# Optimization experiments

Hardware: AMD Instinct MI355X
Metric: run time of the kernel (lower is better)

## Reference

```python
import jax, jax.numpy as jnp
import numpy as np
import math

DIM_V = 512
NUM_HEADS = 8
LN_EPS = 1e-5


def _layer_norm(x, g, b):
    mu = jnp.mean(x, axis=-1, keepdims=True)
    var = jnp.mean(jnp.square(x - mu), axis=-1, keepdims=True)
    return (x - mu) * jax.lax.rsqrt(var + LN_EPS) * g + b


def setup_inputs() -> dict:
    key = jax.random.key(0)
    ks = jax.random.split(key, 12)
    B, Nq, Nk, Dq, Dk, Dv = 16, 1024, 1024, 512, 512, DIM_V
    s_q = 1.0 / math.sqrt(Dq)
    s_k = 1.0 / math.sqrt(Dk)
    s_v = 1.0 / math.sqrt(Dv)
    return {
        "Q": jax.random.normal(ks[0], (B, Nq, Dq), jnp.float32),
        "K": jax.random.normal(ks[1], (B, Nk, Dk), jnp.float32),
        "Wq": jax.random.normal(ks[2], (Dq, Dv), jnp.float32) * s_q,
        "bq": jnp.zeros((Dv,), jnp.float32),
        "Wk": jax.random.normal(ks[3], (Dk, Dv), jnp.float32) * s_k,
        "bk": jnp.zeros((Dv,), jnp.float32),
        "Wv": jax.random.normal(ks[4], (Dk, Dv), jnp.float32) * s_k,
        "bv": jnp.zeros((Dv,), jnp.float32),
        "Wo": jax.random.normal(ks[5], (Dv, Dv), jnp.float32) * s_v,
        "bo": jnp.zeros((Dv,), jnp.float32),
        "g0": jnp.ones((Dv,), jnp.float32),
        "b0": jnp.zeros((Dv,), jnp.float32),
        "g1": jnp.ones((Dv,), jnp.float32),
        "b1": jnp.zeros((Dv,), jnp.float32),
    }


def reference(Q, K, Wq, bq, Wk, bk, Wv, bv, Wo, bo, g0, b0, g1, b1):
    B, Nq, _ = Q.shape
    H = NUM_HEADS
    hd = DIM_V // H
    Qp = Q @ Wq + bq            # [B, Nq, Dv]
    Kp = K @ Wk + bk            # [B, Nk, Dv]
    Vp = K @ Wv + bv            # [B, Nk, Dv]
    # split heads: [B, N, H, hd]
    Qh = Qp.reshape(B, Nq, H, hd)
    Kh = Kp.reshape(B, -1, H, hd)
    Vh = Vp.reshape(B, -1, H, hd)
    # NOTE: original scales by sqrt(dim_V), not sqrt(head_dim)
    scores = jnp.einsum("bqhd,bkhd->bhqk", Qh, Kh) / math.sqrt(DIM_V)
    A = jax.nn.softmax(scores, axis=-1)          # [B, H, Nq, Nk]
    Oh = Qh + jnp.einsum("bhqk,bkhd->bqhd", A, Vh)  # residual on projected Q
    O = Oh.reshape(B, Nq, DIM_V)
    O = _layer_norm(O, g0, b0)
    O = O + jax.nn.relu(O @ Wo + bo)
    O = _layer_norm(O, g1, b1)
    return O
```

## Files before the change

### kernel.cpp

```cpp
#include <hip/hip_runtime.h>
#include <hip/hip_bf16.h>

typedef float f32x4 __attribute__((ext_vector_type(4)));
typedef float f32x16 __attribute__((ext_vector_type(16)));
typedef __bf16 bf16x8 __attribute__((ext_vector_type(8)));
typedef __bf16 bf16x4 __attribute__((ext_vector_type(4)));

#define MFMA(a, b, c) __builtin_amdgcn_mfma_f32_16x16x32_bf16(a, b, c, 0, 0, 0)
#define MFMA32(a, b, c) __builtin_amdgcn_mfma_f32_32x32x16_bf16(a, b, c, 0, 0, 0)
#define AS1 __attribute__((address_space(1)))
#define AS3 __attribute__((address_space(3)))

__device__ __forceinline__ void gload16(const void* g, void* l) {
    __builtin_amdgcn_global_load_lds((const AS1 unsigned int*)g, (AS3 unsigned int*)l, 16, 0, 0);
}

__device__ __forceinline__ unsigned short f2bf(float f) {
    union { float f; unsigned u; } x{f};
    unsigned r = x.u + 0x7FFFu + ((x.u >> 16) & 1u);
    return (unsigned short)(r >> 16);
}
__device__ __forceinline__ float bf2f(unsigned short u) {
    union { unsigned u; float f; } x; x.u = ((unsigned)u) << 16; return x.f;
}
__device__ __forceinline__ unsigned pkbf(float a, float b) {
    union { __bf16 h[2]; unsigned u; } r;
    r.h[0] = (__bf16)a; r.h[1] = (__bf16)b;
    return r.u;
}

__global__ __launch_bounds__(256) void k_transpose4(const float* W0, const float* W1,
                                                    const float* W2, const float* W3,
                                                    unsigned short* T0, unsigned short* T1,
                                                    unsigned short* T2, unsigned short* T3) {
    __shared__ float T[64][65];
    int sel = blockIdx.x >> 6, tile = blockIdx.x & 63;
    const float* W = sel == 0 ? W0 : sel == 1 ? W1 : sel == 2 ? W2 : W3;
    unsigned short* Wt = sel == 0 ? T0 : sel == 1 ? T1 : sel == 2 ? T2 : T3;
    int k0 = (tile >> 3) * 64, n0 = (tile & 7) * 64;
    int tid = threadIdx.x;
    for (int it = 0; it < 16; ++it) {
        int id = it * 256 + tid;
        int r = id >> 6, c = id & 63;
        T[r][c] = W[(k0 + r) * 512 + n0 + c];
    }
    __syncthreads();
    for (int it = 0; it < 16; ++it) {
        int id = it * 256 + tid;
        int r = id >> 6, c = id & 63;
        Wt[(n0 + r) * 512 + k0 + c] = f2bf(T[c][r]);
    }
}

template <int MODE>
__global__ __launch_bounds__(256) void k_gemmF(const float* __restrict__ A,
                                               const unsigned short* __restrict__ Bt,
                                               const float* __restrict__ bias,
                                               void* __restrict__ outp,
                                               float scale) {
    __shared__ __align__(16) float AbS[2][4096];
    __shared__ __align__(16) unsigned short BbS[2][4096];
    const int tid = threadIdx.x;
    const int lane = tid & 63, w = tid >> 6;
    int ib = blockIdx.x;
    const int mt = (ib & 7) | ((ib >> 5) << 3), nt = (ib >> 3) & 3;
    const int m0 = mt * 128, n0 = nt * 128;
    const int wm = (w >> 1) * 64, wn = (w & 1) * 64;
    const int l15 = lane & 15, l4 = lane >> 4;

    const f32x4 vz = {0.f, 0.f, 0.f, 0.f};
    f32x4 acc[4][4];
    for (int i = 0; i < 4; ++i)
        for (int j = 0; j < 4; ++j) acc[i][j] = vz;

    const float* Abase = A + (size_t)m0 * 512;
    const unsigned short* Bbase = Bt + (size_t)n0 * 512;

    auto STAGE = [&](int ks, int p) {
        int kk = ks * 32;
        #pragma unroll
        for (int it = 0; it < 4; ++it) {
            int id = it * 256 + tid;
            int r = id >> 3, cc = id & 7, g = cc ^ (r & 7);
            gload16(Abase + r * 512 + kk + g * 4, &AbS[p][(it * 256 + w * 64) * 4]);
        }
        #pragma unroll
        for (int it = 0; it < 2; ++it) {
            int id = it * 256 + tid;
            int r = id >> 2, x = id & 3, c = x ^ (r & 3);
            gload16(Bbase + r * 512 + kk + c * 8, &BbS[p][(it * 256 + w * 64) * 8]);
        }
    };

    STAGE(0, 0);
    __syncthreads();
    for (int ks = 0; ks < 16; ++ks) {
        int p = ks & 1;
        if (ks < 15) STAGE(ks + 1, p ^ 1);
        bf16x8 af[4], bfr[4];
        #pragma unroll
        for (int i = 0; i < 4; ++i) {
            int r = wm + i * 16 + l15;
            int pc0 = (2 * l4) ^ (r & 7);
            const float* Af = &AbS[p][r * 32];
            f32x4 a0 = *(const f32x4*)(Af + pc0 * 4);
            f32x4 a1 = *(const f32x4*)(Af + (pc0 ^ 1) * 4);
            af[i] = bf16x8{(__bf16)a0[0], (__bf16)a0[1], (__bf16)a0[2], (__bf16)a0[3],
                           (__bf16)a1[0], (__bf16)a1[1], (__bf16)a1[2], (__bf16)a1[3]};
        }
        #pragma unroll
        for (int j = 0; j < 4; ++j) {
            int r = wn + j * 16 + l15, pc = l4 ^ (r & 3);
            bfr[j] = *(const bf16x8*)&BbS[p][r * 32 + pc * 8];
        }
        __builtin_amdgcn_s_setprio(1);
        #pragma unroll
        for (int i = 0; i < 4; ++i)
            #pragma unroll
            for (int j = 0; j < 4; ++j)
                acc[i][j] = MFMA(af[i], bfr[j], acc[i][j]);
        __builtin_amdgcn_s_setprio(0);
        __syncthreads();
    }

    float bn[4];
    for (int j = 0; j < 4; ++j) bn[j] = bias[n0 + wn + j * 16 + l15];

    if constexpr (MODE == 0) {
        unsigned short* out = (unsigned short*)outp;
        for (int i = 0; i < 4; ++i)
            for (int j = 0; j < 4; ++j)
                for (int rg = 0; rg < 4; ++rg) {
                    int m = m0 + wm + i * 16 + l4 * 4 + rg;
                    int n = n0 + wn + j * 16 + l15;
                    out[(size_t)m * 512 + n] = f2bf((acc[i][j][rg] + bn[j]) * scale);
                }
    } else {
        unsigned short* T = (unsigned short*)&AbS[0][0] + w * 4096;
        __syncthreads();
        for (int i = 0; i < 4; ++i)
            for (int j = 0; j < 4; ++j)
                for (int rg = 0; rg < 4; ++rg) {
                    int ml = i * 16 + l4 * 4 + rg;
                    int nl = j * 16 + l15;
                    int pc = (ml >> 3) ^ (nl & 7);
                    T[nl * 64 + pc * 8 + (ml & 7)] = f2bf(acc[i][j][rg] + bn[j]);
                }
        unsigned short* out = (unsigned short*)outp;
        int b = (m0 + wm) >> 10;
        int key0 = (m0 + wm) & 1023;
        for (int it = 0; it < 8; ++it) {
            int ch = it * 64 + lane;
            int nl = ch >> 3, c = ch & 7, pc = c ^ (nl & 7);
            int4 v = *(const int4*)&T[nl * 64 + pc * 8];
            int d = n0 + wn + nl;
            *(int4*)(out + ((size_t)b * 512 + d) * 1024 + key0 + c * 8) = v;
        }
    }
}

__global__ __launch_bounds__(256, 4) void k_attn32(const unsigned short* __restrict__ Qs,
                                                   const unsigned short* __restrict__ Kp,
                                                   const unsigned short* __restrict__ VpT,
                                                   unsigned short* __restrict__ O1b) {
    __shared__ __align__(16) unsigned short sm[16384];
    const int tid = threadIdx.x, lane = tid & 63, w = tid >> 6;
    const int l31 = lane & 31, hi = lane >> 5;
    int i = blockIdx.x;
    const int xcd = i & 7, jj = i >> 3;
    const int qt = jj & 7, bhl = jj >> 3;
    const int bh = xcd * 16 + bhl;
    const int h = bh & 7, b = bh >> 3;
    const int qrow = b * 1024 + qt * 128 + w * 32 + l31;

    const unsigned short* Ksrc = Kp + (size_t)(b * 1024) * 512 + h * 64;
    const unsigned short* Vsrc = VpT + (size_t)(b * 512 + h * 64) * 1024;
    const unsigned short* qptr = Qs + (size_t)qrow * 512 + h * 64;

    bf16x8 qf[4];
    #pragma unroll
    for (int ks = 0; ks < 4; ++ks)
        qf[ks] = *(const bf16x8*)(qptr + ks * 16 + hi * 8);

    f32x16 acc0, acc1;
    #pragma unroll
    for (int r = 0; r < 16; ++r) { acc0[r] = 0.f; acc1[r] = 0.f; }
    float ls = 0.f;

    auto STAGE = [&](int kv, int p) {
        #pragma unroll
        for (int it = 0; it < 2; ++it) {
            int id = it * 256 + tid;
            int r = id >> 3, x = id & 7, c = x ^ (r & 7);
            unsigned short* ldsb = sm + p * 4096 + (it * 256 + w * 64) * 8;
            gload16(Ksrc + (size_t)(kv * 64 + r) * 512 + c * 8, ldsb);
            gload16(Vsrc + (size_t)r * 1024 + kv * 64 + c * 8, ldsb + 8192);
        }
    };

    STAGE(0, 0);
    __syncthreads();
    for (int kv = 0; kv < 16; ++kv) {
        int p = kv & 1;
        if (kv < 15) STAGE(kv + 1, p ^ 1);
        const unsigned short* Kl = sm + p * 4096;
        const unsigned short* Vl = sm + 8192 + p * 4096;
        const int rsw = (l31 & 7);

        f32x16 s0, s1;
        #pragma unroll
        for (int r = 0; r < 16; ++r) { s0[r] = 0.f; s1[r] = 0.f; }
        __builtin_amdgcn_s_setprio(1);
        #pragma unroll
        for (int ks = 0; ks < 4; ++ks) {
            int c = (2 * ks + hi) ^ rsw;
            bf16x8 kf0 = *(const bf16x8*)&Kl[l31 * 64 + c * 8];
            s0 = MFMA32(kf0, qf[ks], s0);
            bf16x8 kf1 = *(const bf16x8*)&Kl[(32 + l31) * 64 + c * 8];
            s1 = MFMA32(kf1, qf[ks], s1);
        }
        __builtin_amdgcn_s_setprio(0);

        unsigned We[8], Wf[8];
        #pragma unroll
        for (int g = 0; g < 4; ++g) {
            float e0 = __builtin_amdgcn_exp2f(s0[4 * g + 0]);
            float e1 = __builtin_amdgcn_exp2f(s0[4 * g + 1]);
            float e2 = __builtin_amdgcn_exp2f(s0[4 * g + 2]);
            float e3 = __builtin_amdgcn_exp2f(s0[4 * g + 3]);
            float f0 = __builtin_amdgcn_exp2f(s1[4 * g + 0]);
            float f1 = __builtin_amdgcn_exp2f(s1[4 * g + 1]);
            float f2 = __builtin_amdgcn_exp2f(s1[4 * g + 2]);
            float f3 = __builtin_amdgcn_exp2f(s1[4 * g + 3]);
            ls += ((e0 + e1) + (e2 + e3)) + ((f0 + f1) + (f2 + f3));
            We[2 * g + 0] = pkbf(e0, e1); We[2 * g + 1] = pkbf(e2, e3);
            Wf[2 * g + 0] = pkbf(f0, f1); Wf[2 * g + 1] = pkbf(f2, f3);
        }
        bf16x8 pf[4];
        #pragma unroll
        for (int src = 0; src < 2; ++src) {
            const unsigned* W = src == 0 ? We : Wf;
            #pragma unroll
            for (int k2 = 0; k2 < 2; ++k2) {
                unsigned A0 = W[4 * k2 + 0], A1 = W[4 * k2 + 1];
                unsigned B0 = W[4 * k2 + 2], B1 = W[4 * k2 + 3];
                unsigned cross0 = __shfl_xor(hi ? A0 : B0, 32);
                unsigned cross1 = __shfl_xor(hi ? A1 : B1, 32);
                union { unsigned w[4]; bf16x8 v; } r;
                r.w[0] = hi ? cross0 : A0;
                r.w[1] = hi ? cross1 : A1;
                r.w[2] = hi ? B0 : cross0;
                r.w[3] = hi ? B1 : cross1;
                pf[src * 2 + k2] = r.v;
            }
        }

        __builtin_amdgcn_s_setprio(1);
        #pragma unroll
        for (int ks = 0; ks < 4; ++ks) {
            int c = (2 * ks + hi) ^ rsw;
            bf16x8 vf0 = *(const bf16x8*)&Vl[l31 * 64 + c * 8];
            acc0 = MFMA32(vf0, pf[ks], acc0);
            bf16x8 vf1 = *(const bf16x8*)&Vl[(32 + l31) * 64 + c * 8];
            acc1 = MFMA32(vf1, pf[ks], acc1);
        }
        __builtin_amdgcn_s_setprio(0);
        __syncthreads();
    }

    ls += __shfl_xor(ls, 32);
    float linv = 1.0f / ls;
    const float invscale = 15.6841306f;
    unsigned short* orow = O1b + (size_t)qrow * 512 + h * 64;
    #pragma unroll
    for (int g = 0; g < 4; ++g) {
        {
            int d0 = 8 * g + 4 * hi;
            bf16x4 qres = *(const bf16x4*)(qptr + d0);
            bf16x4 ov;
            ov[0] = (__bf16)((float)qres[0] * invscale + acc0[4 * g + 0] * linv);
            ov[1] = (__bf16)((float)qres[1] * invscale + acc0[4 * g + 1] * linv);
            ov[2] = (__bf16)((float)qres[2] * invscale + acc0[4 * g + 2] * linv);
            ov[3] = (__bf16)((float)qres[3] * invscale + acc0[4 * g + 3] * linv);
            *(bf16x4*)(orow + d0) = ov;
        }
        {
            int d0 = 32 + 8 * g + 4 * hi;
            bf16x4 qres = *(const bf16x4*)(qptr + d0);
            bf16x4 ov;
            ov[0] = (__bf16)((float)qres[0] * invscale + acc1[4 * g + 0] * linv);
            ov[1] = (__bf16)((float)qres[1] * invscale + acc1[4 * g + 1] * linv);
            ov[2] = (__bf16)((float)qres[2] * invscale + acc1[4 * g + 2] * linv);
            ov[3] = (__bf16)((float)qres[3] * invscale + acc1[4 * g + 3] * linv);
            *(bf16x4*)(orow + d0) = ov;
        }
    }
}

__global__ __launch_bounds__(256) void k_ln_bf(const unsigned short* __restrict__ in,
                                               unsigned short* __restrict__ outb,
                                               const float* __restrict__ g,
                                               const float* __restrict__ bt) {
    int row = blockIdx.x * 4 + (threadIdx.x >> 6);
    int lane = threadIdx.x & 63;
    const unsigned short* x = in + (size_t)row * 512 + lane * 8;
    bf16x8 v = *(const bf16x8*)x;
    float f[8];
    for (int j = 0; j < 8; ++j) f[j] = (float)v[j];
    float s1 = 0.f, s2 = 0.f;
    for (int j = 0; j < 8; ++j) { s1 += f[j]; s2 += f[j] * f[j]; }
    for (int off = 32; off; off >>= 1) {
        s1 += __shfl_xor(s1, off);
        s2 += __shfl_xor(s2, off);
    }
    float mu = s1 * (1.f / 512.f);
    float var = s2 * (1.f / 512.f) - mu * mu;
    float rs = rsqrtf(var + 1e-5f);
    float4 ga = *(const float4*)(g + lane * 8), gb = *(const float4*)(g + lane * 8 + 4);
    float4 ba = *(const float4*)(bt + lane * 8), bb = *(const float4*)(bt + lane * 8 + 4);
    float gg[8] = {ga.x, ga.y, ga.z, ga.w, gb.x, gb.y, gb.z, gb.w};
    float bv[8] = {ba.x, ba.y, ba.z, ba.w, bb.x, bb.y, bb.z, bb.w};
    bf16x8 y;
    for (int j = 0; j < 8; ++j) y[j] = (__bf16)((f[j] - mu) * rs * gg[j] + bv[j]);
    *(bf16x8*)(outb + (size_t)row * 512 + lane * 8) = y;
}

__global__ __launch_bounds__(512, 2) void k_gemm2ln(const unsigned short* __restrict__ A,
                                                    const unsigned short* __restrict__ Bt,
                                                    const float* __restrict__ bias,
                                                    const float* __restrict__ g1,
                                                    const float* __restrict__ b1,
                                                    float* __restrict__ out) {
    __shared__ __align__(16) unsigned short Ab[2][2048];
    __shared__ __align__(16) unsigned short Bb[2][16384];
    __shared__ float part[64][4][2];
    __shared__ float stats[64][2];
    const int tid = threadIdx.x, lane = tid & 63, w = tid >> 6;
    const int l15 = lane & 15, l4 = lane >> 4;
    const int m0 = blockIdx.x * 64;
    const int wm = (w >> 2) * 32, wn = (w & 3) * 128;

    const f32x4 vz = {0.f, 0.f, 0.f, 0.f};
    f32x4 acc[2][8];
    for (int i = 0; i < 2; ++i)
        for (int j = 0; j < 8; ++j) acc[i][j] = vz;

    const unsigned short* Abase = A + (size_t)m0 * 512;

    auto STAGE = [&](int ks, int p) {
        int kk = ks * 32;
        for (int it = 0; it < 4; ++it) {
            int id = it * 512 + tid;
            int r = id >> 2, x = id & 3, c = x ^ (r & 3);
            gload16(Bt + r * 512 + kk + c * 8, &Bb[p][(it * 512 + w * 64) * 8]);
        }
        if (w < 4) {
            int id = w * 64 + lane;
            int r = id >> 2, x = id & 3, c = x ^ (r & 3);
            gload16(Abase + r * 512 + kk + c * 8, &Ab[p][(w * 64) * 8]);
        }
    };

    STAGE(0, 0);
    __syncthreads();
    for (int ks = 0; ks < 16; ++ks) {
        int p = ks & 1;
        if (ks < 15) STAGE(ks + 1, p ^ 1);
        bf16x8 af[2], bfr[8];
        for (int i = 0; i < 2; ++i) {
            int r = wm + i * 16 + l15, pc = l4 ^ (r & 3);
            af[i] = *(const bf16x8*)&Ab[p][r * 32 + pc * 8];
        }
        for (int j = 0; j < 8; ++j) {
            int r = wn + j * 16 + l15, pc = l4 ^ (r & 3);
            bfr[j] = *(const bf16x8*)&Bb[p][r * 32 + pc * 8];
        }
        __builtin_amdgcn_s_setprio(1);
        for (int i = 0; i < 2; ++i)
            for (int j = 0; j < 8; ++j)
                acc[i][j] = MFMA(af[i], bfr[j], acc[i][j]);
        __builtin_amdgcn_s_setprio(0);
        __syncthreads();
    }

    float bn[8], gv[8], bv2[8];
    for (int j = 0; j < 8; ++j) {
        int n = wn + j * 16 + l15;
        bn[j] = bias[n]; gv[j] = g1[n]; bv2[j] = b1[n];
    }
    f32x4 s1v[2], s2v[2];
    for (int i = 0; i < 2; ++i) { s1v[i] = vz; s2v[i] = vz; }
    for (int i = 0; i < 2; ++i)
        for (int j = 0; j < 8; ++j)
            for (int rg = 0; rg < 4; ++rg) {
                int row = m0 + wm + i * 16 + l4 * 4 + rg;
                int n = wn + j * 16 + l15;
                float z = acc[i][j][rg] + bn[j];
                z = z > 0.f ? z : 0.f;
                float v = bf2f(A[(size_t)row * 512 + n]) + z;
                acc[i][j][rg] = v;
                s1v[i][rg] += v;
                s2v[i][rg] += v * v;
            }
    for (int i = 0; i < 2; ++i)
        for (int rg = 0; rg < 4; ++rg) {
            float a = s1v[i][rg], c = s2v[i][rg];
            for (int off = 1; off < 16; off <<= 1) {
                a += __shfl_xor(a, off);
                c += __shfl_xor(c, off);
            }
            s1v[i][rg] = a; s2v[i][rg] = c;
        }
    if (l15 == 0)
        for (int i = 0; i < 2; ++i)
            for (int rg = 0; rg < 4; ++rg) {
                int rl = wm + i * 16 + l4 * 4 + rg;
                part[rl][w & 3][0] = s1v[i][rg];
                part[rl][w & 3][1] = s2v[i][rg];
            }
    __syncthreads();
    if (tid < 64) {
        float a = 0.f, c = 0.f;
        for (int q = 0; q < 4; ++q) { a += part[tid][q][0]; c += part[tid][q][1]; }
        float mu = a * (1.f / 512.f);
        float var = c * (1.f / 512.f) - mu * mu;
        stats[tid][0] = mu;
        stats[tid][1] = rsqrtf(var + 1e-5f);
    }
    __syncthreads();
    for (int i = 0; i < 2; ++i)
        for (int rg = 0; rg < 4; ++rg) {
            int rl = wm + i * 16 + l4 * 4 + rg;
            float mu = stats[rl][0], rs = stats[rl][1];
            for (int j = 0; j < 8; ++j) {
                int n = wn + j * 16 + l15;
                out[(size_t)(m0 + rl) * 512 + n] = (acc[i][j][rg] - mu) * rs * gv[j] + bv2[j];
            }
        }
}

extern "C" void kernel_launch(void* const* d_in, const int* in_sizes, int n_in,
                              void* d_out, int out_size, void* d_ws, size_t ws_size,
                              hipStream_t stream) {
    const float* Q  = (const float*)d_in[0];
    const float* K  = (const float*)d_in[1];
    const float* Wq = (const float*)d_in[2];
    const float* bq = (const float*)d_in[3];
    const float* Wk = (const float*)d_in[4];
    const float* bk = (const float*)d_in[5];
    const float* Wv = (const float*)d_in[6];
    const float* bv = (const float*)d_in[7];
    const float* Wo = (const float*)d_in[8];
    const float* bo = (const float*)d_in[9];
    const float* g0 = (const float*)d_in[10];
    const float* b0 = (const float*)d_in[11];
    const float* g1 = (const float*)d_in[12];
    const float* b1 = (const float*)d_in[13];
    float* out = (float*)d_out;

    const size_t SZ_BF = (size_t)16384 * 512 * 2;
    const size_t SZ_W  = (size_t)512 * 512 * 2;
    char* p = (char*)d_ws;
    unsigned short* Wqt = (unsigned short*)p; p += SZ_W;
    unsigned short* Wkt = (unsigned short*)p; p += SZ_W;
    unsigned short* Wvt = (unsigned short*)p; p += SZ_W;
    unsigned short* Wot = (unsigned short*)p; p += SZ_W;
    unsigned short* Qsc = (unsigned short*)p; p += SZ_BF;
    unsigned short* Kp  = (unsigned short*)p; p += SZ_BF;
    unsigned short* VpT = (unsigned short*)p; p += SZ_BF;
    unsigned short* A1b = (unsigned short*)p; p += SZ_BF;
    unsigned short* X0b = (unsigned short*)p; p += SZ_BF;

    k_transpose4<<<256, 256, 0, stream>>>(Wq, Wk, Wv, Wo, Wqt, Wkt, Wvt, Wot);

    const float scale2 = 0.063758718f;
    k_gemmF<0><<<512, 256, 0, stream>>>(Q, Wqt, bq, Qsc, scale2);
    k_gemmF<0><<<512, 256, 0, stream>>>(K, Wkt, bk, Kp, 1.0f);
    k_gemmF<1><<<512, 256, 0, stream>>>(K, Wvt, bv, VpT, 1.0f);

    k_attn32<<<1024, 256, 0, stream>>>(Qsc, Kp, VpT, A1b);

    k_ln_bf<<<4096, 256, 0, stream>>>(A1b, X0b, g0, b0);
    k_gemm2ln<<<256, 512, 0, stream>>>(X0b, Wot, bo, g1, b1, out);
}
```

Baseline: 154.6 us.

## Merge QKV projections into one launch; attention waves process 64 query rows

Folds the three projection GEMM launches into a single 1536-block kernel that picks its input, weights and output by block index, which removes launch gaps and fills the device better. The attention kernel moves to 128-thread blocks where each wave handles two 32-row query groups, so every K/V fragment read from LDS feeds twice as many MFMAs. Each block also starts its KV loop at a rotated tile offset so concurrent blocks read different K/V tiles. In exchange the attention kernel uses more registers per wave and has fewer waves per block to hide load latency.

Result: faster. 142.5 us (-7.8%).

```diff
diff --git a/kernel.cpp b/kernel.cpp
--- a/kernel.cpp
+++ b/kernel.cpp
@@ -27,6 +27,42 @@
     union { __bf16 h[2]; unsigned u; } r;
     r.h[0] = (__bf16)a; r.h[1] = (__bf16)b;
     return r.u;
+}
+
+__device__ __forceinline__ void softmax_pack(const f32x16& s0, const f32x16& s1,
+                                             float& ls, int hi, bf16x8* pf) {
+    unsigned We[8], Wf[8];
+    #pragma unroll
+    for (int g = 0; g < 4; ++g) {
+        float e0 = __builtin_amdgcn_exp2f(s0[4 * g + 0]);
+        float e1 = __builtin_amdgcn_exp2f(s0[4 * g + 1]);
+        float e2 = __builtin_amdgcn_exp2f(s0[4 * g + 2]);
+        float e3 = __builtin_amdgcn_exp2f(s0[4 * g + 3]);
+        float f0 = __builtin_amdgcn_exp2f(s1[4 * g + 0]);
+        float f1 = __builtin_amdgcn_exp2f(s1[4 * g + 1]);
+        float f2 = __builtin_amdgcn_exp2f(s1[4 * g + 2]);
+        float f3 = __builtin_amdgcn_exp2f(s1[4 * g + 3]);
+        ls += ((e0 + e1) + (e2 + e3)) + ((f0 + f1) + (f2 + f3));
+        We[2 * g + 0] = pkbf(e0, e1); We[2 * g + 1] = pkbf(e2, e3);
+        Wf[2 * g + 0] = pkbf(f0, f1); Wf[2 * g + 1] = pkbf(f2, f3);
+    }
+    #pragma unroll
+    for (int src = 0; src < 2; ++src) {
+        const unsigned* W = src == 0 ? We : Wf;
+        #pragma unroll
+        for (int k2 = 0; k2 < 2; ++k2) {
+            unsigned A0 = W[4 * k2 + 0], A1 = W[4 * k2 + 1];
+            unsigned B0 = W[4 * k2 + 2], B1 = W[4 * k2 + 3];
+            unsigned cross0 = __shfl_xor(hi ? A0 : B0, 32);
+            unsigned cross1 = __shfl_xor(hi ? A1 : B1, 32);
+            union { unsigned w[4]; bf16x8 v; } r;
+            r.w[0] = hi ? cross0 : A0;
+            r.w[1] = hi ? cross1 : A1;
+            r.w[2] = hi ? B0 : cross0;
+            r.w[3] = hi ? B1 : cross1;
+            pf[src * 2 + k2] = r.v;
+        }
+    }
 }
 
 __global__ __launch_bounds__(256) void k_transpose4(const float* W0, const float* W1,
@@ -52,17 +88,28 @@
     }
 }
 
-template <int MODE>
-__global__ __launch_bounds__(256) void k_gemmF(const float* __restrict__ A,
-                                               const unsigned short* __restrict__ Bt,
-                                               const float* __restrict__ bias,
-                                               void* __restrict__ outp,
-                                               float scale) {
+__global__ __launch_bounds__(256) void k_proj(const float* __restrict__ Qf,
+                                              const float* __restrict__ Kf,
+                                              const unsigned short* __restrict__ Wqt,
+                                              const unsigned short* __restrict__ Wkt,
+                                              const unsigned short* __restrict__ Wvt,
+                                              const float* __restrict__ bq,
+                                              const float* __restrict__ bk,
+                                              const float* __restrict__ bv,
+                                              unsigned short* __restrict__ Qsc,
+                                              unsigned short* __restrict__ Kpo,
+                                              unsigned short* __restrict__ VpT,
+                                              float scale2) {
     __shared__ __align__(16) float AbS[2][4096];
     __shared__ __align__(16) unsigned short BbS[2][4096];
     const int tid = threadIdx.x;
     const int lane = tid & 63, w = tid >> 6;
-    int ib = blockIdx.x;
+    const int sel = blockIdx.x >> 9;
+    int ib = blockIdx.x & 511;
+    const float* A = sel == 0 ? Qf : Kf;
+    const unsigned short* Bt = sel == 0 ? Wqt : sel == 1 ? Wkt : Wvt;
+    const float* bias = sel == 0 ? bq : sel == 1 ? bk : bv;
+    const float scale = sel == 0 ? scale2 : 1.0f;
     const int mt = (ib & 7) | ((ib >> 5) << 3), nt = (ib >> 3) & 3;
     const int m0 = mt * 128, n0 = nt * 128;
     const int wm = (w >> 1) * 64, wn = (w & 1) * 64;
@@ -126,8 +173,8 @@
     float bn[4];
     for (int j = 0; j < 4; ++j) bn[j] = bias[n0 + wn + j * 16 + l15];
 
-    if constexpr (MODE == 0) {
-        unsigned short* out = (unsigned short*)outp;
+    if (sel < 2) {
+        unsigned short* out = sel == 0 ? Qsc : Kpo;
         for (int i = 0; i < 4; ++i)
             for (int j = 0; j < 4; ++j)
                 for (int rg = 0; rg < 4; ++rg) {
@@ -146,7 +193,6 @@
                     int pc = (ml >> 3) ^ (nl & 7);
                     T[nl * 64 + pc * 8 + (ml & 7)] = f2bf(acc[i][j][rg] + bn[j]);
                 }
-        unsigned short* out = (unsigned short*)outp;
         int b = (m0 + wm) >> 10;
         int key0 = (m0 + wm) & 1023;
         for (int it = 0; it < 8; ++it) {
@@ -154,12 +200,12 @@
             int nl = ch >> 3, c = ch & 7, pc = c ^ (nl & 7);
             int4 v = *(const int4*)&T[nl * 64 + pc * 8];
             int d = n0 + wn + nl;
-            *(int4*)(out + ((size_t)b * 512 + d) * 1024 + key0 + c * 8) = v;
-        }
-    }
-}
-
-__global__ __launch_bounds__(256, 4) void k_attn32(const unsigned short* __restrict__ Qs,
+            *(int4*)(VpT + ((size_t)b * 512 + d) * 1024 + key0 + c * 8) = v;
+        }
+    }
+}
+
+__global__ __launch_bounds__(128, 2) void k_attn64(const unsigned short* __restrict__ Qs,
                                                    const unsigned short* __restrict__ Kp,
                                                    const unsigned short* __restrict__ VpT,
                                                    unsigned short* __restrict__ O1b) {
@@ -167,132 +213,125 @@
     const int tid = threadIdx.x, lane = tid & 63, w = tid >> 6;
     const int l31 = lane & 31, hi = lane >> 5;
     int i = blockIdx.x;
-    const int xcd = i & 7, jj = i >> 3;
-    const int qt = jj & 7, bhl = jj >> 3;
+    const int xcd = i & 7, r2 = i >> 3;
+    const int bhl = r2 & 15, qt = r2 >> 4;
     const int bh = xcd * 16 + bhl;
     const int h = bh & 7, b = bh >> 3;
-    const int qrow = b * 1024 + qt * 128 + w * 32 + l31;
+    const int q0 = b * 1024 + qt * 128 + w * 64;
+    const int kv0 = (qt * 3 + bhl * 5) & 15;
 
     const unsigned short* Ksrc = Kp + (size_t)(b * 1024) * 512 + h * 64;
     const unsigned short* Vsrc = VpT + (size_t)(b * 512 + h * 64) * 1024;
-    const unsigned short* qptr = Qs + (size_t)qrow * 512 + h * 64;
-
-    bf16x8 qf[4];
+    const unsigned short* qptrA = Qs + (size_t)(q0 + l31) * 512 + h * 64;
+    const unsigned short* qptrB = qptrA + (size_t)32 * 512;
+
+    bf16x8 qfA[4], qfB[4];
     #pragma unroll
-    for (int ks = 0; ks < 4; ++ks)
-        qf[ks] = *(const bf16x8*)(qptr + ks * 16 + hi * 8);
-
-    f32x16 acc0, acc1;
+    for (int ks = 0; ks < 4; ++ks) {
+        qfA[ks] = *(const bf16x8*)(qptrA + ks * 16 + hi * 8);
+        qfB[ks] = *(const bf16x8*)(qptrB + ks * 16 + hi * 8);
+    }
+
+    f32x16 accA0, accA1, accB0, accB1;
     #pragma unroll
-    for (int r = 0; r < 16; ++r) { acc0[r] = 0.f; acc1[r] = 0.f; }
-    float ls = 0.f;
-
-    auto STAGE = [&](int kv, int p) {
-        #pragma unroll
-        for (int it = 0; it < 2; ++it) {
-            int id = it * 256 + tid;
+    for (int r = 0; r < 16; ++r) { accA0[r] = 0.f; accA1[r] = 0.f; accB0[r] = 0.f; accB1[r] = 0.f; }
+    float lsA = 0.f, lsB = 0.f;
+
+    auto STAGE = [&](int j, int p) {
+        int t = (j + kv0) & 15;
+        #pragma unroll
+        for (int it = 0; it < 4; ++it) {
+            int id = it * 128 + tid;
             int r = id >> 3, x = id & 7, c = x ^ (r & 7);
-            unsigned short* ldsb = sm + p * 4096 + (it * 256 + w * 64) * 8;
-            gload16(Ksrc + (size_t)(kv * 64 + r) * 512 + c * 8, ldsb);
-            gload16(Vsrc + (size_t)r * 1024 + kv * 64 + c * 8, ldsb + 8192);
+            unsigned short* kb = sm + p * 4096 + (it * 128 + w * 64) * 8;
+            gload16(Ksrc + (size_t)(t * 64 + r) * 512 + c * 8, kb);
+            gload16(Vsrc + (size_t)r * 1024 + t * 64 + c * 8, kb + 8192);
         }
     };
 
     STAGE(0, 0);
     __syncthreads();
-    for (int kv = 0; kv < 16; ++kv) {
-        int p = kv & 1;
-        if (kv < 15) STAGE(kv + 1, p ^ 1);
+    const int rsw = l31 & 7;
+    for (int it2 = 0; it2 < 16; ++it2) {
+        int p = it2 & 1;
+        if (it2 < 15) STAGE(it2 + 1, p ^ 1);
         const unsigned short* Kl = sm + p * 4096;
         const unsigned short* Vl = sm + 8192 + p * 4096;
-        const int rsw = (l31 & 7);
-
-        f32x16 s0, s1;
-        #pragma unroll
-        for (int r = 0; r < 16; ++r) { s0[r] = 0.f; s1[r] = 0.f; }
+
+        f32x16 s0a, s1a, s0b, s1b;
+        #pragma unroll
+        for (int r = 0; r < 16; ++r) { s0a[r] = 0.f; s1a[r] = 0.f; s0b[r] = 0.f; s1b[r] = 0.f; }
         __builtin_amdgcn_s_setprio(1);
         #pragma unroll
         for (int ks = 0; ks < 4; ++ks) {
             int c = (2 * ks + hi) ^ rsw;
             bf16x8 kf0 = *(const bf16x8*)&Kl[l31 * 64 + c * 8];
-            s0 = MFMA32(kf0, qf[ks], s0);
             bf16x8 kf1 = *(const bf16x8*)&Kl[(32 + l31) * 64 + c * 8];
-            s1 = MFMA32(kf1, qf[ks], s1);
+            s0a = MFMA32(kf0, qfA[ks], s0a);
+            s1a = MFMA32(kf1, qfA[ks], s1a);
+            s0b = MFMA32(kf0, qfB[ks], s0b);
+            s1b = MFMA32(kf1, qfB[ks], s1b);
         }
         __builtin_amdgcn_s_setprio(0);
 
-        unsigned We[8], Wf[8];
-        #pragma unroll
-        for (int g = 0; g < 4; ++g) {
-            float e0 = __builtin_amdgcn_exp2f(s0[4 * g + 0]);
-            float e1 = __builtin_amdgcn_exp2f(s0[4 * g + 1]);
-            float e2 = __builtin_amdgcn_exp2f(s0[4 * g + 2]);
-            float e3 = __builtin_amdgcn_exp2f(s0[4 * g + 3]);
-            float f0 = __builtin_amdgcn_exp2f(s1[4 * g + 0]);
-            float f1 = __builtin_amdgcn_exp2f(s1[4 * g + 1]);
-            float f2 = __builtin_amdgcn_exp2f(s1[4 * g + 2]);
-            float f3 = __builtin_amdgcn_exp2f(s1[4 * g + 3]);
-            ls += ((e0 + e1) + (e2 + e3)) + ((f0 + f1) + (f2 + f3));
-            We[2 * g + 0] = pkbf(e0, e1); We[2 * g + 1] = pkbf(e2, e3);
-            Wf[2 * g + 0] = pkbf(f0, f1); Wf[2 * g + 1] = pkbf(f2, f3);
-        }
-        bf16x8 pf[4];
-        #pragma unroll
-        for (int src = 0; src < 2; ++src) {
-            const unsigned* W = src == 0 ? We : Wf;
-            #pragma unroll
-            for (int k2 = 0; k2 < 2; ++k2) {
-                unsigned A0 = W[4 * k2 + 0], A1 = W[4 * k2 + 1];
-                unsigned B0 = W[4 * k2 + 2], B1 = W[4 * k2 + 3];
-                unsigned cross0 = __shfl_xor(hi ? A0 : B0, 32);
-                unsigned cross1 = __shfl_xor(hi ? A1 : B1, 32);
-                union { unsigned w[4]; bf16x8 v; } r;
-                r.w[0] = hi ? cross0 : A0;
-                r.w[1] = hi ? cross1 : A1;
-                r.w[2] = hi ? B0 : cross0;
-                r.w[3] = hi ? B1 : cross1;
-                pf[src * 2 + k2] = r.v;
-            }
-        }
+        bf16x8 pfA[4], pfB[4];
+        softmax_pack(s0a, s1a, lsA, hi, pfA);
+        softmax_pack(s0b, s1b, lsB, hi, pfB);
 
         __builtin_amdgcn_s_setprio(1);
         #pragma unroll
         for (int ks = 0; ks < 4; ++ks) {
             int c = (2 * ks + hi) ^ rsw;
             bf16x8 vf0 = *(const bf16x8*)&Vl[l31 * 64 + c * 8];
-            acc0 = MFMA32(vf0, pf[ks], acc0);
             bf16x8 vf1 = *(const bf16x8*)&Vl[(32 + l31) * 64 + c * 8];
-            acc1 = MFMA32(vf1, pf[ks], acc1);
+            accA0 = MFMA32(vf0, pfA[ks], accA0);
+            accA1 = MFMA32(vf1, pfA[ks], accA1);
+            accB0 = MFMA32(vf0, pfB[ks], accB0);
+            accB1 = MFMA32(vf1, pfB[ks], accB1);
         }
         __builtin_amdgcn_s_setprio(0);
         __syncthreads();
     }
 
-    ls += __shfl_xor(ls, 32);
-    float linv = 1.0f / ls;
     const float invscale = 15.6841306f;
-    unsigned short* orow = O1b + (size_t)qrow * 512 + h * 64;
-    #pragma unroll
-    for (int g = 0; g < 4; ++g) {
-        {
+    {
+        float l = lsA + __shfl_xor(lsA, 32);
+        float linv = 1.0f / l;
+        unsigned short* orow = O1b + (size_t)(q0 + l31) * 512 + h * 64;
+        #pragma unroll
+        for (int g = 0; g < 4; ++g) {
             int d0 = 8 * g + 4 * hi;
-            bf16x4 qres = *(const bf16x4*)(qptr + d0);
+            bf16x4 qres = *(const bf16x4*)(qptrA + d0);
             bf16x4 ov;
-            ov[0] = (__bf16)((float)qres[0] * invscale + acc0[4 * g + 0] * linv);
-            ov[1] = (__bf16)((float)qres[1] * invscale + acc0[4 * g + 1] * linv);
-            ov[2] = (__bf16)((float)qres[2] * invscale + acc0[4 * g + 2] * linv);
-            ov[3] = (__bf16)((float)qres[3] * invscale + acc0[4 * g + 3] * linv);
+            for (int j = 0; j < 4; ++j)
+                ov[j] = (__bf16)((float)qres[j] * invscale + accA0[4 * g + j] * linv);
             *(bf16x4*)(orow + d0) = ov;
-        }
-        {
-            int d0 = 32 + 8 * g + 4 * hi;
-            bf16x4 qres = *(const bf16x4*)(qptr + d0);
+            int d1 = 32 + d0;
+            bf16x4 qres1 = *(const bf16x4*)(qptrA + d1);
+            bf16x4 ov1;
+            for (int j = 0; j < 4; ++j)
+                ov1[j] = (__bf16)((float)qres1[j] * invscale + accA1[4 * g + j] * linv);
+            *(bf16x4*)(orow + d1) = ov1;
+        }
+    }
+    {
+        float l = lsB + __shfl_xor(lsB, 32);
+        float linv = 1.0f / l;
+        unsigned short* orow = O1b + (size_t)(q0 + 32 + l31) * 512 + h * 64;
+        #pragma unroll
+        for (int g = 0; g < 4; ++g) {
+            int d0 = 8 * g + 4 * hi;
+            bf16x4 qres = *(const bf16x4*)(qptrB + d0);
             bf16x4 ov;
-            ov[0] = (__bf16)((float)qres[0] * invscale + acc1[4 * g + 0] * linv);
-            ov[1] = (__bf16)((float)qres[1] * invscale + acc1[4 * g + 1] * linv);
-            ov[2] = (__bf16)((float)qres[2] * invscale + acc1[4 * g + 2] * linv);
-            ov[3] = (__bf16)((float)qres[3] * invscale + acc1[4 * g + 3] * linv);
+            for (int j = 0; j < 4; ++j)
+                ov[j] = (__bf16)((float)qres[j] * invscale + accB0[4 * g + j] * linv);
             *(bf16x4*)(orow + d0) = ov;
+            int d1 = 32 + d0;
+            bf16x4 qres1 = *(const bf16x4*)(qptrB + d1);
+            bf16x4 ov1;
+            for (int j = 0; j < 4; ++j)
+                ov1[j] = (__bf16)((float)qres1[j] * invscale + accB1[4 * g + j] * linv);
+            *(bf16x4*)(orow + d1) = ov1;
         }
     }
 }
@@ -474,11 +513,9 @@
     k_transpose4<<<256, 256, 0, stream>>>(Wq, Wk, Wv, Wo, Wqt, Wkt, Wvt, Wot);
 
     const float scale2 = 0.063758718f;
-    k_gemmF<0><<<512, 256, 0, stream>>>(Q, Wqt, bq, Qsc, scale2);
-    k_gemmF<0><<<512, 256, 0, stream>>>(K, Wkt, bk, Kp, 1.0f);
-    k_gemmF<1><<<512, 256, 0, stream>>>(K, Wvt, bv, VpT, 1.0f);
-
-    k_attn32<<<1024, 256, 0, stream>>>(Qsc, Kp, VpT, A1b);
+    k_proj<<<1536, 256, 0, stream>>>(Q, K, Wqt, Wkt, Wvt, bq, bk, bv, Qsc, Kp, VpT, scale2);
+
+    k_attn64<<<1024, 128, 0, stream>>>(Qsc, Kp, VpT, A1b);
 
     k_ln_bf<<<4096, 256, 0, stream>>>(A1b, X0b, g0, b0);
     k_gemm2ln<<<256, 512, 0, stream>>>(X0b, Wot, bo, g1, b1, out);
```
